# Optimization experiments

Measured on AMD Instinct MI355X. Metric: run time of the kernel, lower is better.

Reference implementation:

```python
import jax, jax.numpy as jnp
import numpy as np
from jax import lax

B, CIN, COUT, H, W = 8, 256, 128, 64, 64
KK = 9  # 3x3 kernel positions
EPS = 1e-5


def setup_inputs() -> dict:
    key = jax.random.key(0)
    ks = jax.random.split(key, 6)
    x = jax.random.normal(ks[0], (B, CIN, H, W), jnp.float32)
    # DCNv2 offset/mask conv: 3*kk channels (9 dy, 9 dx, 9 mask logits); init near zero as in DCN
    w_off = jax.random.normal(ks[1], (3 * KK, CIN, 3, 3), jnp.float32) * 0.01
    b_off = jnp.zeros((3 * KK,), jnp.float32)
    w_dcn = jax.random.normal(ks[2], (COUT, CIN, 3, 3), jnp.float32) * (1.0 / np.sqrt(CIN * 9))
    b_dcn = jnp.zeros((COUT,), jnp.float32)
    gamma1 = jnp.ones((COUT,), jnp.float32)
    beta1 = jnp.zeros((COUT,), jnp.float32)
    # torch ConvTranspose2d weight layout: [in, out, kh, kw]
    w_ct = jax.random.normal(ks[3], (COUT, COUT, 4, 4), jnp.float32) * (1.0 / np.sqrt(COUT * 16))
    gamma2 = jnp.ones((COUT,), jnp.float32)
    beta2 = jnp.zeros((COUT,), jnp.float32)
    return dict(x=x, w_off=w_off, b_off=b_off, w_dcn=w_dcn, b_dcn=b_dcn,
                gamma1=gamma1, beta1=beta1, w_ct=w_ct, gamma2=gamma2, beta2=beta2)


def _bn_relu(x, g, b):
    # BatchNorm2d (training mode: batch stats, biased var) + ReLU
    mu = jnp.mean(x, axis=(0, 2, 3), keepdims=True)
    var = jnp.var(x, axis=(0, 2, 3), keepdims=True)
    y = (x - mu) * lax.rsqrt(var + EPS) * g[None, :, None, None] + b[None, :, None, None]
    return jax.nn.relu(y)


def _forward(x, w_off, b_off, w_dcn, b_dcn, gamma1, beta1, w_ct, gamma2, beta2):
    Bx, C, Hx, Wx = x.shape
    dn = ('NCHW', 'OIHW', 'NCHW')
    # --- DCNv2: offset/mask conv (3x3, stride 1, pad 1) ---
    om = lax.conv_general_dilated(x, w_off, (1, 1), ((1, 1), (1, 1)), dimension_numbers=dn)
    om = om + b_off[None, :, None, None]
    o_y, o_x, m = om[:, :KK], om[:, KK:2 * KK], om[:, 2 * KK:]
    mask = jax.nn.sigmoid(m)  # [B,9,H,W]
    # base sampling grid: p = p0 - pad + k*dilation + offset
    ky, kx = jnp.meshgrid(jnp.arange(3, dtype=x.dtype), jnp.arange(3, dtype=x.dtype), indexing='ij')
    ky, kx = ky.reshape(KK), kx.reshape(KK)
    py = o_y + (jnp.arange(Hx, dtype=x.dtype)[None, :, None] - 1.0 + ky[:, None, None])[None]  # [B,9,H,W]
    px = o_x + (jnp.arange(Wx, dtype=x.dtype)[None, None, :] - 1.0 + kx[:, None, None])[None]
    y0 = jnp.floor(py)
    x0 = jnp.floor(px)
    ly = py - y0
    lx = px - x0
    xf = x.reshape(Bx, C, Hx * Wx)

    def corner(yi, xi, wgt):
        valid = (yi >= 0) & (yi < Hx) & (xi >= 0) & (xi < Wx)  # zero padding outside
        idx = (jnp.clip(yi, 0, Hx - 1).astype(jnp.int32) * Wx
               + jnp.clip(xi, 0, Wx - 1).astype(jnp.int32))  # [B,9,H,W]
        v = jax.vmap(lambda xb, ib: xb[:, ib])(xf, idx.reshape(Bx, -1))  # [B,C,9*H*W]
        v = v.reshape(Bx, C, KK, Hx, Wx)
        return v * (wgt * valid)[:, None]

    sampled = (corner(y0, x0, (1 - ly) * (1 - lx))
               + corner(y0, x0 + 1, (1 - ly) * lx)
               + corner(y0 + 1, x0, ly * (1 - lx))
               + corner(y0 + 1, x0 + 1, ly * lx))  # [B,C,9,H,W]
    sampled = sampled * mask[:, None]  # modulated (DCNv2)
    out = jnp.einsum('bckhw,ock->bohw', sampled, w_dcn.reshape(w_dcn.shape[0], C, KK))
    out = out + b_dcn[None, :, None, None]
    out = _bn_relu(out, gamma1, beta1)
    # --- ConvTranspose2d(k=4, s=2, p=1): conv with lhs_dilation=2, pad=k-1-p=2, flipped kernel ---
    wt = jnp.flip(w_ct, (2, 3)).transpose(1, 0, 2, 3)  # [out,in,4,4]
    out2 = lax.conv_general_dilated(out, wt, (1, 1), ((2, 2), (2, 2)),
                                    lhs_dilation=(2, 2), dimension_numbers=dn)
    return _bn_relu(out2, gamma2, beta2)  # [B,COUT,2H,2W]


def reference(x, w_off, b_off, w_dcn, b_dcn, gamma1, beta1, w_ct, gamma2, beta2):
    return _forward(x, w_off, b_off, w_dcn, b_dcn, gamma1, beta1, w_ct, gamma2, beta2)
```

## Files before the change

### kernel.cpp

```cpp
#include <hip/hip_runtime.h>
#include <stdint.h>

__device__ int   g_isf32;
__device__ float g_stats[512];

typedef __attribute__((ext_vector_type(8))) short bf16x8;
typedef __attribute__((ext_vector_type(4))) float f32x4;

__device__ __forceinline__ float bf2f(unsigned short u) {
  union { unsigned int i; float f; } v; v.i = ((unsigned int)u) << 16; return v.f;
}
__device__ __forceinline__ unsigned short f2bf(float f) {
  union { float f; unsigned int i; } v; v.f = f;
  unsigned int r = v.i + 0x7FFFu + ((v.i >> 16) & 1u);
  return (unsigned short)(r >> 16);
}
__device__ __forceinline__ unsigned int pk2(float a, float b) {
  return (unsigned int)f2bf(a) | ((unsigned int)f2bf(b) << 16);
}
__device__ __forceinline__ float ldi(const void* p, size_t i, int f) {
  return f ? ((const float*)p)[i] : bf2f(((const unsigned short*)p)[i]);
}

__global__ void k_detect(const unsigned short* __restrict__ x) {
  __shared__ int cnt;
  const int t = threadIdx.x;
  if (t == 0) cnt = 0;
  g_stats[t] = 0.f; g_stats[t + 256] = 0.f;
  __syncthreads();
  int c = 0;
  for (int j = 0; j < 16; j++) {
    unsigned short u = x[t * 16 + j];
    int e = (u >> 7) & 0xFF;
    if (e == 0xFF || (e != 0 && e <= 100)) c++;
  }
  atomicAdd(&cnt, c);
  __syncthreads();
  if (t == 0) g_isf32 = (cnt > 256) ? 1 : 0;
}

__global__ void k_prep(const void* __restrict__ w_dcn, const void* __restrict__ w_ct,
                       const void* __restrict__ w_off,
                       float* __restrict__ wdcnT, float* __restrict__ wctT,
                       float* __restrict__ woffT, unsigned short* __restrict__ wdcnA,
                       unsigned short* __restrict__ woffA) {
  const int f = g_isf32;
  int idx = blockIdx.x * 256 + threadIdx.x;
  if (idx < 294912) {
    int k = idx / 32768, c = (idx >> 7) & 255, o = idx & 127;
    wdcnT[idx] = ldi(w_dcn, (size_t)(o * 256 + c) * 9 + k, f);
  }
  int i2 = idx - 294912;
  if (i2 >= 0 && i2 < 262144) {
    int kr = i2 >> 16, kc = (i2 >> 14) & 3, i = (i2 >> 7) & 127, o = i2 & 127;
    wctT[i2] = ldi(w_ct, (size_t)((i * 128 + o) * 4 + kr) * 4 + kc, f);
  }
  int i3 = idx - (294912 + 262144);
  if (i3 >= 0 && i3 < 62208) {
    int ci = i3 / 243, r = i3 - ci * 243, k = r / 27, c = r - (r / 27) * 27;
    woffT[i3] = ldi(w_off, (size_t)(c * 256 + ci) * 9 + k, f);
  }
  int i4 = idx - 619264;
  if (i4 >= 0 && i4 < 294912) {
    int o = i4 / 2304, rem = i4 - o * 2304;
    int k = rem >> 8, c = rem & 255;
    wdcnA[i4] = f2bf(ldi(w_dcn, (size_t)(o * 256 + c) * 9 + k, f));
  }
  int i5 = idx - 914176;
  if (i5 >= 0 && i5 < 73728) {
    int m = i5 / 2304, r = i5 - m * 2304;
    int tap = r >> 8, ci = r & 255;
    float v = (m < 27) ? ldi(w_off, (size_t)(m * 256 + ci) * 9 + tap, f) : 0.f;
    woffA[i5] = f2bf(v);
  }
}

__global__ void k_prep2(const float* __restrict__ wctT, unsigned short* __restrict__ Apar) {
  int idx = blockIdx.x * 256 + threadIdx.x;
  int par = idx >> 16, rem = idx & 65535;
  int o = rem >> 9, rem2 = rem & 511;
  int tap = rem2 >> 7, i = rem2 & 127;
  int py = par >> 1, px = par & 1, a = tap >> 1, bb = tap & 1;
  int kr = (py == 0) ? (a ? 3 : 1) : (a ? 2 : 0);
  int kc = (px == 0) ? (bb ? 3 : 1) : (bb ? 2 : 0);
  Apar[idx] = f2bf(wctT[((size_t)(kr * 4 + kc) * 128 + i) * 128 + o]);
}

__global__ __launch_bounds__(256) void k_xt(const void* __restrict__ x,
                                            unsigned short* __restrict__ xT) {
  const int f = g_isf32;
  const int h = blockIdx.x, cq = blockIdx.y, b = blockIdx.z;
  const int t = threadIdx.x;
  __shared__ unsigned short T[64][72];
  {
    int cl = t >> 2, q = t & 3;
    size_t base = ((size_t)((b * 256 + cq * 64 + cl) * 64 + h) << 6) + q * 16;
    unsigned short r[16];
    if (f) {
      const float4* p = (const float4*)((const float*)x + base);
      float4 v0 = p[0], v1 = p[1], v2 = p[2], v3 = p[3];
      float vv[16] = {v0.x, v0.y, v0.z, v0.w, v1.x, v1.y, v1.z, v1.w,
                      v2.x, v2.y, v2.z, v2.w, v3.x, v3.y, v3.z, v3.w};
#pragma unroll
      for (int j = 0; j < 16; j++) r[j] = f2bf(vv[j]);
    } else {
      const unsigned short* p = (const unsigned short*)x + base;
      *(uint4*)&r[0] = *(const uint4*)p;
      *(uint4*)&r[8] = *(const uint4*)(p + 8);
    }
    *(uint4*)&T[cl][q * 16]     = *(uint4*)&r[0];
    *(uint4*)&T[cl][q * 16 + 8] = *(uint4*)&r[8];
  }
  __syncthreads();
  {
    int pl = t >> 2, qc = t & 3;
    unsigned short r[16];
#pragma unroll
    for (int j = 0; j < 16; j++) r[j] = T[qc * 16 + j][pl];
    unsigned short* op = xT + ((size_t)((b * 64 + h) * 64 + pl) << 8) + cq * 64 + qc * 16;
    *(uint4*)op       = *(uint4*)&r[0];
    *(uint4*)(op + 8) = *(uint4*)&r[8];
  }
}

__global__ __launch_bounds__(256) void k_offmfma(
    const unsigned short* __restrict__ xT,
    const unsigned short* __restrict__ woffA,
    const void* __restrict__ b_off, float* __restrict__ om) {
  const int f = g_isf32;
  const int h = blockIdx.x, b = blockIdx.y;
  const int t = threadIdx.x;
  const int wv = t >> 6, L = t & 63, quad = L >> 4, l15 = L & 15;
  __shared__ unsigned short Bs[3][66][40];
  f32x4 acc[2] = {};
  const int sl = t >> 6, sw = t & 63;

  for (int cq = 0; cq < 8; cq++) {
    __syncthreads();
    if (t < 192) {
      int row = h - 1 + sl;
      uint4 q0 = make_uint4(0, 0, 0, 0), q1 = q0, q2 = q0, q3 = q0;
      if (row >= 0 && row < 64) {
        const unsigned short* src = xT + ((size_t)((b * 64 + row) * 64 + sw) << 8) + cq * 32;
        q0 = *(const uint4*)(src);
        q1 = *(const uint4*)(src + 8);
        q2 = *(const uint4*)(src + 16);
        q3 = *(const uint4*)(src + 24);
      }
      unsigned short* d = &Bs[sl][sw + 1][0];
      *(uint4*)(d)      = q0; *(uint4*)(d + 8)  = q1;
      *(uint4*)(d + 16) = q2; *(uint4*)(d + 24) = q3;
    } else if (t < 198) {
      int idx = t - 192;
      int zs = idx >> 1, zc = (idx & 1) ? 65 : 0;
      unsigned short* d = &Bs[zs][zc][0];
      uint4 z = make_uint4(0, 0, 0, 0);
      *(uint4*)(d) = z; *(uint4*)(d + 8) = z; *(uint4*)(d + 16) = z; *(uint4*)(d + 24) = z;
    }
    __syncthreads();
#pragma unroll
    for (int tap = 0; tap < 9; tap++) {
      const int dy = tap / 3, dx = tap - dy * 3;
      const int kb = tap * 256 + cq * 32 + quad * 8;
      bf16x8 a0 = *(const bf16x8*)(woffA + (size_t)l15 * 2304 + kb);
      bf16x8 a1 = *(const bf16x8*)(woffA + (size_t)(l15 + 16) * 2304 + kb);
      bf16x8 bv = *(const bf16x8*)&Bs[dy][wv * 16 + l15 + dx][quad * 8];
      acc[0] = __builtin_amdgcn_mfma_f32_16x16x32_bf16(a0, bv, acc[0], 0, 0, 0);
      acc[1] = __builtin_amdgcn_mfma_f32_16x16x32_bf16(a1, bv, acc[1], 0, 0, 0);
    }
  }
  const int w = wv * 16 + l15;
#pragma unroll
  for (int tm = 0; tm < 2; tm++) {
#pragma unroll
    for (int r = 0; r < 4; r++) {
      int m = tm * 16 + quad * 4 + r;
      if (m < 27) {
        float bo = ldi(b_off, m, f);
        om[(size_t)((b * 27 + m) * 64 + h) * 64 + w] = acc[tm][r] + bo;
      }
    }
  }
}

__global__ __launch_bounds__(256) void k_offconv(
    const void* __restrict__ x, const void* __restrict__ b_off,
    const float* __restrict__ woffT, float* __restrict__ om) {
  const int f = g_isf32;
  const int h = blockIdx.x, b = blockIdx.y;
  const int t = threadIdx.x;
  const int cg = t & 31, wg = t >> 5;
  const int w0 = wg * 8;
  __shared__ float xs[32 * 204];
  float acc[8];
#pragma unroll
  for (int i = 0; i < 8; i++) acc[i] = 0.f;

  for (int cb = 0; cb < 256; cb += 32) {
    __syncthreads();
    for (int e = t; e < 32 * 192; e += 256) {
      int ci = e / 192, r = e - ci * 192;
      int dh = r >> 6, w = r & 63;
      int row = h + dh - 1;
      float v = 0.f;
      if (row >= 0 && row < 64)
        v = ldi(x, ((size_t)((b * 256 + cb + ci) * 64 + row) << 6) + w, f);
      xs[ci * 204 + dh * 68 + w + 1] = v;
    }
    for (int e = t; e < 96; e += 256) {
      int base = (e / 3) * 204 + (e - (e / 3) * 3) * 68;
      xs[base] = 0.f; xs[base + 65] = 0.f; xs[base + 66] = 0.f; xs[base + 67] = 0.f;
    }
    __syncthreads();

    for (int ci = 0; ci < 32; ci++) {
      float xr[3][12];
#pragma unroll
      for (int dh = 0; dh < 3; dh++) {
        const float* p = &xs[ci * 204 + dh * 68 + w0];
        float4 q0 = *(const float4*)(p);
        float4 q1 = *(const float4*)(p + 4);
        float4 q2 = *(const float4*)(p + 8);
        xr[dh][0] = q0.x; xr[dh][1] = q0.y; xr[dh][2] = q0.z; xr[dh][3] = q0.w;
        xr[dh][4] = q1.x; xr[dh][5] = q1.y; xr[dh][6] = q1.z; xr[dh][7] = q1.w;
        xr[dh][8] = q2.x; xr[dh][9] = q2.y; xr[dh][10] = q2.z; xr[dh][11] = q2.w;
      }
      if (cg < 27) {
        const float* wp = &woffT[(size_t)(cb + ci) * 243 + cg];
#pragma unroll
        for (int k = 0; k < 9; k++) {
          float wk = wp[k * 27];
          const int dh = k / 3, dx = k - (k / 3) * 3;
#pragma unroll
          for (int wi = 0; wi < 8; wi++)
            acc[wi] = fmaf(wk, xr[dh][wi + dx], acc[wi]);
        }
      }
    }
  }
  if (cg < 27) {
    float bo = ldi(b_off, cg, f);
    float* op = &om[(size_t)((b * 27 + cg) * 64 + h) * 64 + w0];
#pragma unroll
    for (int wi = 0; wi < 8; wi++) op[wi] = acc[wi] + bo;
  }
}

__global__ __launch_bounds__(256) void k_dcnf(
    const unsigned short* __restrict__ xT,
    const unsigned short* __restrict__ A,
    const float* __restrict__ om,
    const void* __restrict__ b_dcn,
    unsigned short* __restrict__ h1) {
  const int f = g_isf32;
  const int b = blockIdx.x, nt = blockIdx.y;
  const int t = threadIdx.x;
  const int wv = t >> 6, L = t & 63, quad = L >> 4, l15 = L & 15;
  const int wm = wv * 32;
  __shared__ unsigned short As[128][40];
  __shared__ unsigned short Bs[32][40];
  __shared__ float          Wg[9][32][4];
  __shared__ unsigned short Wi[9][32][4];
  f32x4 acc[2][2] = {};
  const int p0 = nt * 32;

  for (int e = t; e < 9 * 32; e += 256) {
    int k = e >> 5, p = e & 31;
    int pos = p0 + p;
    int hh = pos >> 6, ww = pos & 63;
    const float* ob = om + (size_t)(b * 27) * 4096 + pos;
    float oy = ob[(size_t)k * 4096];
    float ox = ob[(size_t)(k + 9) * 4096];
    float mm = ob[(size_t)(k + 18) * 4096];
    float msk = 1.f / (1.f + expf(-mm));
    float py = oy + (float)(hh - 1 + k / 3);
    float px = ox + (float)(ww - 1 + (k - (k / 3) * 3));
    float y0f = floorf(py), x0f = floorf(px);
    float ly = py - y0f, lx = px - x0f;
    int y0 = (int)y0f, x0 = (int)x0f;
    int y1 = y0 + 1, x1 = x0 + 1;
    float fy0 = (y0 >= 0 && y0 < 64) ? 1.f : 0.f;
    float fy1 = (y1 >= 0 && y1 < 64) ? 1.f : 0.f;
    float fx0 = (x0 >= 0 && x0 < 64) ? 1.f : 0.f;
    float fx1 = (x1 >= 0 && x1 < 64) ? 1.f : 0.f;
    int y0c = min(max(y0, 0), 63), y1c = min(max(y1, 0), 63);
    int x0c = min(max(x0, 0), 63), x1c = min(max(x1, 0), 63);
    Wg[k][p][0] = (1.f - ly) * (1.f - lx) * msk * fy0 * fx0;
    Wg[k][p][1] = (1.f - ly) * lx * msk * fy0 * fx1;
    Wg[k][p][2] = ly * (1.f - lx) * msk * fy1 * fx0;
    Wg[k][p][3] = ly * lx * msk * fy1 * fx1;
    Wi[k][p][0] = (unsigned short)(y0c * 64 + x0c);
    Wi[k][p][1] = (unsigned short)(y0c * 64 + x1c);
    Wi[k][p][2] = (unsigned short)(y1c * 64 + x0c);
    Wi[k][p][3] = (unsigned short)(y1c * 64 + x1c);
  }
  __syncthreads();

  const unsigned short* xb = xT + ((size_t)b << 20);
  const int sp = t >> 3, qc8 = t & 7;
  const int am = t >> 1, aseg = t & 1;
  const unsigned short* aprow = A + (size_t)am * 2304 + aseg * 16;

  uint4 pa0, pa1;
  uint2 pu0, pu1, pu2, pu3;
  float4 pg;

#define DCNF_ISSUE(S) {                                                   \
    int tap_ = (S) >> 3, cq_ = (S) & 7;                                   \
    int kb_ = tap_ * 256 + cq_ * 32;                                      \
    pa0 = *(const uint4*)(aprow + kb_);                                   \
    pa1 = *(const uint4*)(aprow + kb_ + 8);                               \
    pg  = *(const float4*)&Wg[tap_][sp][0];                               \
    uint2 wi2_ = *(const uint2*)&Wi[tap_][sp][0];                         \
    int i0_ = wi2_.x & 0xffff, i1_ = wi2_.x >> 16;                        \
    int i2_ = wi2_.y & 0xffff, i3_ = wi2_.y >> 16;                        \
    int cb_ = cq_ * 32 + qc8 * 4;                                         \
    pu0 = *(const uint2*)(xb + ((size_t)i0_ << 8) + cb_);                 \
    pu1 = *(const uint2*)(xb + ((size_t)i1_ << 8) + cb_);                 \
    pu2 = *(const uint2*)(xb + ((size_t)i2_ << 8) + cb_);                 \
    pu3 = *(const uint2*)(xb + ((size_t)i3_ << 8) + cb_);                 \
  }

  DCNF_ISSUE(0);
  for (int s = 0; s < 72; s++) {
    __syncthreads();
    *(uint4*)&As[am][aseg * 16]     = pa0;
    *(uint4*)&As[am][aseg * 16 + 8] = pa1;
    {
      unsigned short e0[4], e1[4], e2[4], e3[4];
      *(uint2*)e0 = pu0; *(uint2*)e1 = pu1; *(uint2*)e2 = pu2; *(uint2*)e3 = pu3;
      float g0 = pg.x, g1 = pg.y, g2 = pg.z, g3 = pg.w;
      unsigned int r[2];
#pragma unroll
      for (int j = 0; j < 2; j++) {
        float va = g0 * bf2f(e0[2 * j])     + g1 * bf2f(e1[2 * j])
                 + g2 * bf2f(e2[2 * j])     + g3 * bf2f(e3[2 * j]);
        float vb = g0 * bf2f(e0[2 * j + 1]) + g1 * bf2f(e1[2 * j + 1])
                 + g2 * bf2f(e2[2 * j + 1]) + g3 * bf2f(e3[2 * j + 1]);
        r[j] = pk2(va, vb);
      }
      *(uint2*)&Bs[sp][qc8 * 4] = make_uint2(r[0], r[1]);
    }
    if (s < 71) DCNF_ISSUE(s + 1);
    __syncthreads();
    const int ar = quad * 8;
    bf16x8 af[2], bfr[2];
#pragma unroll
    for (int tm = 0; tm < 2; tm++) af[tm]  = *(const bf16x8*)&As[wm + tm * 16 + l15][ar];
#pragma unroll
    for (int tn = 0; tn < 2; tn++) bfr[tn] = *(const bf16x8*)&Bs[tn * 16 + l15][ar];
#pragma unroll
    for (int tm = 0; tm < 2; tm++)
#pragma unroll
      for (int tn = 0; tn < 2; tn++)
        acc[tm][tn] = __builtin_amdgcn_mfma_f32_16x16x32_bf16(af[tm], bfr[tn], acc[tm][tn], 0, 0, 0);
  }
#undef DCNF_ISSUE

#pragma unroll
  for (int tm = 0; tm < 2; tm++) {
#pragma unroll
    for (int r = 0; r < 4; r++) {
      int m = wm + tm * 16 + quad * 4 + r;
      float bd = ldi(b_dcn, m, f);
#pragma unroll
      for (int tn = 0; tn < 2; tn++) {
        float v = acc[tm][tn][r] + bd;
        int n = p0 + tn * 16 + l15;
        h1[(size_t)(b * 128 + m) * 4096 + n] = f2bf(v);
      }
    }
  }
}

__global__ __launch_bounds__(256) void k_stats1(const unsigned short* __restrict__ h1) {
  const int m = blockIdx.x, b = blockIdx.y;
  const int t = threadIdx.x;
  const unsigned short* p = h1 + (size_t)(b * 128 + m) * 4096 + t * 16;
  uint4 q0 = *(const uint4*)p;
  uint4 q1 = *(const uint4*)(p + 8);
  unsigned short e[16];
  *(uint4*)&e[0] = q0; *(uint4*)&e[8] = q1;
  float s = 0.f, q = 0.f;
#pragma unroll
  for (int j = 0; j < 16; j++) { float v = bf2f(e[j]); s += v; q += v * v; }
#pragma unroll
  for (int msk = 1; msk < 64; msk <<= 1) {
    s += __shfl_xor(s, msk, 64);
    q += __shfl_xor(q, msk, 64);
  }
  if ((t & 63) == 0) { atomicAdd(&g_stats[m], s); atomicAdd(&g_stats[128 + m], q); }
}

__global__ __launch_bounds__(256) void k_dcn(
    const void* __restrict__ x, const float* __restrict__ om,
    const float* __restrict__ wdcnT, const void* __restrict__ b_dcn,
    unsigned short* __restrict__ h1) {
  const int f = g_isf32;
  const int h = blockIdx.x, b = blockIdx.y;
  const int t = threadIdx.x;
  __shared__ float S[64 * 64];
  __shared__ int   midx[64][4];
  __shared__ float mwgt[64][4];
  const int og = t >> 4, pg = t & 15;
  const int pA = t & 63, cgA = t >> 6;
  float acc[8][4];
#pragma unroll
  for (int j = 0; j < 8; j++)
#pragma unroll
    for (int i = 0; i < 4; i++) acc[j][i] = 0.f;

  for (int k = 0; k < 9; k++) {
    if (t < 64) {
      const int w = t;
      const float* ob = &om[(size_t)(b * 27) * 4096 + h * 64 + w];
      float oy = ob[(size_t)k * 4096];
      float ox = ob[(size_t)(k + 9) * 4096];
      float mm = ob[(size_t)(k + 18) * 4096];
      float msk = 1.f / (1.f + expf(-mm));
      float py = oy + (float)(h - 1 + k / 3);
      float px = ox + (float)(w - 1 + (k - (k / 3) * 3));
      float y0f = floorf(py), x0f = floorf(px);
      float ly = py - y0f, lx = px - x0f;
      int y0 = (int)y0f, x0 = (int)x0f;
      int y1 = y0 + 1, x1 = x0 + 1;
      float fy0 = (y0 >= 0 && y0 < 64) ? 1.f : 0.f;
      float fy1 = (y1 >= 0 && y1 < 64) ? 1.f : 0.f;
      float fx0 = (x0 >= 0 && x0 < 64) ? 1.f : 0.f;
      float fx1 = (x1 >= 0 && x1 < 64) ? 1.f : 0.f;
      int y0c = min(max(y0, 0), 63), y1c = min(max(y1, 0), 63);
      int x0c = min(max(x0, 0), 63), x1c = min(max(x1, 0), 63);
      midx[w][0] = y0c * 64 + x0c;
      midx[w][1] = y0c * 64 + x1c;
      midx[w][2] = y1c * 64 + x0c;
      midx[w][3] = y1c * 64 + x1c;
      mwgt[w][0] = (1.f - ly) * (1.f - lx) * msk * fy0 * fx0;
      mwgt[w][1] = (1.f - ly) * lx * msk * fy0 * fx1;
      mwgt[w][2] = ly * (1.f - lx) * msk * fy1 * fx0;
      mwgt[w][3] = ly * lx * msk * fy1 * fx1;
    }
    for (int ch = 0; ch < 4; ch++) {
      __syncthreads();
      {
        const int i0 = midx[pA][0], i1 = midx[pA][1], i2 = midx[pA][2], i3 = midx[pA][3];
        const float g0 = mwgt[pA][0], g1 = mwgt[pA][1], g2 = mwgt[pA][2], g3 = mwgt[pA][3];
        const size_t cbase = (size_t)(b * 256 + ch * 64 + cgA * 16) * 4096;
        float* Sp = &S[(cgA * 16) * 64 + pA];
#pragma unroll 4
        for (int j = 0; j < 16; j++) {
          const size_t xo = cbase + (size_t)j * 4096;
          float v = g0 * ldi(x, xo + i0, f) + g1 * ldi(x, xo + i1, f)
                  + g2 * ldi(x, xo + i2, f) + g3 * ldi(x, xo + i3, f);
          Sp[j * 64] = v;
        }
      }
      __syncthreads();
      const float* wk = wdcnT + (size_t)k * 32768 + (size_t)(ch * 64) * 128;
#pragma unroll 2
      for (int c2 = 0; c2 < 64; c2++) {
        float4 a0 = *(const float4*)&wk[c2 * 128 + og * 8];
        float4 a1 = *(const float4*)&wk[c2 * 128 + og * 8 + 4];
        float4 s4 = *(const float4*)&S[c2 * 64 + pg * 4];
        float aa[8] = {a0.x, a0.y, a0.z, a0.w, a1.x, a1.y, a1.z, a1.w};
        float ss[4] = {s4.x, s4.y, s4.z, s4.w};
#pragma unroll
        for (int j = 0; j < 8; j++)
#pragma unroll
          for (int i = 0; i < 4; i++)
            acc[j][i] = fmaf(aa[j], ss[i], acc[j][i]);
      }
    }
  }
#pragma unroll
  for (int j = 0; j < 8; j++) {
    const int o = og * 8 + j;
    float bd = ldi(b_dcn, o, f);
    float v0 = acc[j][0] + bd, v1 = acc[j][1] + bd, v2 = acc[j][2] + bd, v3 = acc[j][3] + bd;
    float s = v0 + v1 + v2 + v3;
    float q = v0 * v0 + v1 * v1 + v2 * v2 + v3 * v3;
    uint2 pkv = make_uint2(pk2(v0, v1), pk2(v2, v3));
    *(uint2*)(h1 + (size_t)((b * 128 + o) * 64 + h) * 64 + pg * 4) = pkv;
#pragma unroll
    for (int m = 1; m < 16; m <<= 1) {
      s += __shfl_xor(s, m, 64);
      q += __shfl_xor(q, m, 64);
    }
    if (pg == 0) { atomicAdd(&g_stats[o], s); atomicAdd(&g_stats[128 + o], q); }
  }
}

__global__ __launch_bounds__(256) void k_bn1t(
    const unsigned short* __restrict__ h1, const void* __restrict__ g1,
    const void* __restrict__ be1, unsigned short* __restrict__ h1T) {
  const int f = g_isf32;
  const int pt = blockIdx.x, chh = blockIdx.y, b = blockIdx.z;
  const int t = threadIdx.x;
  __shared__ unsigned short T[64][72];
  const int c0 = chh * 64, p0 = pt * 64;
  {
    int cl = t >> 2, q = t & 3;
    int o = c0 + cl;
    float mu = g_stats[o] * (1.f / 32768.f);
    float var = g_stats[128 + o] * (1.f / 32768.f) - mu * mu;
    float sc = rsqrtf(var + 1e-5f) * ldi(g1, o, f);
    float sh = ldi(be1, o, f) - mu * sc;
    const unsigned short* hp = h1 + (size_t)(b * 128 + o) * 4096 + p0 + q * 16;
    uint4 q0 = *(const uint4*)hp, q1 = *(const uint4*)(hp + 8);
    unsigned short e[16], r[16];
    *(uint4*)&e[0] = q0; *(uint4*)&e[8] = q1;
#pragma unroll
    for (int j = 0; j < 16; j++)
      r[j] = f2bf(fmaxf(fmaf(bf2f(e[j]), sc, sh), 0.f));
    *(uint4*)&T[cl][q * 16]     = *(uint4*)&r[0];
    *(uint4*)&T[cl][q * 16 + 8] = *(uint4*)&r[8];
  }
  __syncthreads();
  {
    int pl = t >> 2, qc = t & 3;
    unsigned short r[16];
#pragma unroll
    for (int j = 0; j < 16; j++) r[j] = T[qc * 16 + j][pl];
    unsigned short* op = h1T + (size_t)(b * 4096 + p0 + pl) * 128 + c0 + qc * 16;
    *(uint4*)op       = *(uint4*)&r[0];
    *(uint4*)(op + 8) = *(uint4*)&r[8];
  }
}

__global__ void k_bn1(unsigned short* __restrict__ h1, const void* __restrict__ g1,
                      const void* __restrict__ be1) {
  const int f = g_isf32;
  int gid = blockIdx.x * 256 + threadIdx.x;
  size_t base = (size_t)gid * 8;
  int o = (int)((base >> 12) & 127);
  float mu = g_stats[o] * (1.f / 32768.f);
  float var = g_stats[128 + o] * (1.f / 32768.f) - mu * mu;
  float sc = rsqrtf(var + 1e-5f) * ldi(g1, o, f);
  float sh = ldi(be1, o, f) - mu * sc;
  uint4 p = *(const uint4*)(h1 + base);
  unsigned int pp[4] = {p.x, p.y, p.z, p.w};
  unsigned int r[4];
#pragma unroll
  for (int i = 0; i < 4; i++) {
    float f0 = fmaxf(fmaf(bf2f((unsigned short)(pp[i] & 0xffff)), sc, sh), 0.f);
    float f1 = fmaxf(fmaf(bf2f((unsigned short)(pp[i] >> 16)), sc, sh), 0.f);
    r[i] = pk2(f0, f1);
  }
  *(uint4*)(h1 + base) = make_uint4(r[0], r[1], r[2], r[3]);
}

__global__ __launch_bounds__(256) void k_ctgemm(
    const unsigned short* __restrict__ h1T,
    const unsigned short* __restrict__ Apar,
    void* __restrict__ out2p) {
  const int f = g_isf32;
  const int nt = blockIdx.x, par = blockIdx.y, b = blockIdx.z;
  const int py = par >> 1, px = par & 1;
  const int t = threadIdx.x;
  const int wv = t >> 6, L = t & 63;
  const int quad = L >> 4, l15 = L & 15;
  const int wm = (wv >> 1) * 64, wn = (wv & 1) * 64;
  __shared__ unsigned short As[128][40];
  __shared__ unsigned short Bs[128][40];
  f32x4 acc[4][4] = {};
  const int y0 = nt * 2;
  const unsigned short* Ap = Apar + (size_t)par * 128 * 512;
  const unsigned short* hb = h1T + (size_t)b * 4096 * 128;
  const int sp = t >> 1, shalf = t & 1;
  const int srr = sp >> 6, sx = sp & 63;

  for (int kk = 0; kk < 512; kk += 32) {
    const int tap = kk >> 7, ic = kk & 127;
    const int a = tap >> 1, bb = tap & 1;
    const int ya = (py == 0) ? (a ? -1 : 0) : (a ? 0 : 1);
    const int xb = (px == 0) ? (bb ? -1 : 0) : (bb ? 0 : 1);
    __syncthreads();
    {
      int m = t >> 1, seg = t & 1;
      const unsigned short* ap = Ap + (size_t)m * 512 + kk + seg * 16;
      uint4 q0 = *(const uint4*)(ap);
      uint4 q1 = *(const uint4*)(ap + 8);
      *(uint4*)&As[m][seg * 16]     = q0;
      *(uint4*)&As[m][seg * 16 + 8] = q1;
    }
    {
      int srcy = y0 + srr + ya;
      int srcx = sx + xb;
      uint4 q0 = make_uint4(0, 0, 0, 0), q1 = q0;
      if (srcy >= 0 && srcy < 64 && srcx >= 0 && srcx < 64) {
        const unsigned short* hp = hb + ((size_t)(srcy * 64 + srcx)) * 128 + ic + shalf * 16;
        q0 = *(const uint4*)(hp);
        q1 = *(const uint4*)(hp + 8);
      }
      *(uint4*)&Bs[sp][shalf * 16]     = q0;
      *(uint4*)&Bs[sp][shalf * 16 + 8] = q1;
    }
    __syncthreads();
    const int ar = quad * 8;
    bf16x8 af[4], bfr[4];
#pragma unroll
    for (int tm = 0; tm < 4; tm++) af[tm]  = *(const bf16x8*)&As[wm + tm * 16 + l15][ar];
#pragma unroll
    for (int tn = 0; tn < 4; tn++) bfr[tn] = *(const bf16x8*)&Bs[wn + tn * 16 + l15][ar];
#pragma unroll
    for (int tm = 0; tm < 4; tm++)
#pragma unroll
      for (int tn = 0; tn < 4; tn++)
        acc[tm][tn] = __builtin_amdgcn_mfma_f32_16x16x32_bf16(af[tm], bfr[tn], acc[tm][tn], 0, 0, 0);
  }

  const size_t obase = (size_t)((par * 8 + b) * 128) * 4096;
#pragma unroll
  for (int tm = 0; tm < 4; tm++) {
#pragma unroll
    for (int r = 0; r < 4; r++) {
      int m = wm + tm * 16 + quad * 4 + r;
#pragma unroll
      for (int tn = 0; tn < 4; tn++) {
        float v = acc[tm][tn][r];
        int n = wn + tn * 16 + l15;
        size_t ofs = obase + (size_t)m * 4096 + (size_t)((y0 + (n >> 6)) * 64 + (n & 63));
        if (f) ((float*)out2p)[ofs] = v;
        else   ((unsigned short*)out2p)[ofs] = f2bf(v);
      }
    }
  }
}

__global__ __launch_bounds__(256) void k_stats2(const void* __restrict__ out2p) {
  const int f = g_isf32;
  const int m = blockIdx.x, pb = blockIdx.y;
  const int t = threadIdx.x;
  size_t base = ((size_t)pb * 128 + m) * 4096 + (size_t)t * 16;
  float s = 0.f, q = 0.f;
  if (f) {
    const float* p = (const float*)out2p + base;
#pragma unroll
    for (int j = 0; j < 4; j++) {
      float4 v = *(const float4*)(p + j * 4);
      s += v.x + v.y + v.z + v.w;
      q += v.x * v.x + v.y * v.y + v.z * v.z + v.w * v.w;
    }
  } else {
    const unsigned short* p = (const unsigned short*)out2p + base;
    uint4 q0 = *(const uint4*)p, q1 = *(const uint4*)(p + 8);
    unsigned short e[16];
    *(uint4*)&e[0] = q0; *(uint4*)&e[8] = q1;
#pragma unroll
    for (int j = 0; j < 16; j++) { float v = bf2f(e[j]); s += v; q += v * v; }
  }
#pragma unroll
  for (int msk = 1; msk < 64; msk <<= 1) {
    s += __shfl_xor(s, msk, 64);
    q += __shfl_xor(q, msk, 64);
  }
  if ((t & 63) == 0) { atomicAdd(&g_stats[256 + m], s); atomicAdd(&g_stats[384 + m], q); }
}

__global__ __launch_bounds__(256) void k_bn2f(
    const void* __restrict__ out2p, const void* __restrict__ g2,
    const void* __restrict__ be2, void* __restrict__ out) {
  const int f = g_isf32;
  const int m = blockIdx.x, b = blockIdx.y;
  const int t = threadIdx.x;
  float mu = g_stats[256 + m] * (1.f / 131072.f);
  float var = g_stats[384 + m] * (1.f / 131072.f) - mu * mu;
  float sc = rsqrtf(var + 1e-5f) * ldi(g2, m, f);
  float sh = ldi(be2, m, f) - mu * sc;
  const int row8 = t >> 3, xseg = t & 7;
  const int xh0 = xseg * 8;
#pragma unroll
  for (int pss = 0; pss < 4; pss++) {
    int yy = pss * 32 + row8;
    int y = yy >> 1, py = yy & 1;
    size_t s0 = ((size_t)((py * 2 + 0) * 8 + b) * 128 + m) * 4096 + (size_t)(y * 64 + xh0);
    size_t s1 = ((size_t)((py * 2 + 1) * 8 + b) * 128 + m) * 4096 + (size_t)(y * 64 + xh0);
    float v0[8], v1[8];
    if (f) {
      const float* p0 = (const float*)out2p + s0;
      const float* p1 = (const float*)out2p + s1;
      float4 a0 = *(const float4*)p0, a1 = *(const float4*)(p0 + 4);
      float4 c0 = *(const float4*)p1, c1 = *(const float4*)(p1 + 4);
      v0[0] = a0.x; v0[1] = a0.y; v0[2] = a0.z; v0[3] = a0.w;
      v0[4] = a1.x; v0[5] = a1.y; v0[6] = a1.z; v0[7] = a1.w;
      v1[0] = c0.x; v1[1] = c0.y; v1[2] = c0.z; v1[3] = c0.w;
      v1[4] = c1.x; v1[5] = c1.y; v1[6] = c1.z; v1[7] = c1.w;
    } else {
      const unsigned short* p0 = (const unsigned short*)out2p + s0;
      const unsigned short* p1 = (const unsigned short*)out2p + s1;
      uint4 u0 = *(const uint4*)p0, u1 = *(const uint4*)p1;
      unsigned short e0[8], e1[8];
      *(uint4*)&e0[0] = u0; *(uint4*)&e1[0] = u1;
#pragma unroll
      for (int j = 0; j < 8; j++) { v0[j] = bf2f(e0[j]); v1[j] = bf2f(e1[j]); }
    }
    float r[16];
#pragma unroll
    for (int i = 0; i < 8; i++) {
      r[2 * i]     = fmaxf(fmaf(v0[i], sc, sh), 0.f);
      r[2 * i + 1] = fmaxf(fmaf(v1[i], sc, sh), 0.f);
    }
    size_t ob = (size_t)(b * 128 + m) * 16384 + (size_t)yy * 128 + (size_t)(xh0 * 2);
    if (f) {
      float* op = (float*)out + ob;
#pragma unroll
      for (int v4 = 0; v4 < 4; v4++)
        ((float4*)op)[v4] = make_float4(r[4 * v4], r[4 * v4 + 1], r[4 * v4 + 2], r[4 * v4 + 3]);
    } else {
      unsigned short* op = (unsigned short*)out + ob;
      unsigned int w_[8];
#pragma unroll
      for (int i = 0; i < 8; i++) w_[i] = pk2(r[2 * i], r[2 * i + 1]);
      *(uint4*)(op)     = make_uint4(w_[0], w_[1], w_[2], w_[3]);
      *(uint4*)(op + 8) = make_uint4(w_[4], w_[5], w_[6], w_[7]);
    }
  }
}

__global__ __launch_bounds__(256) void k_ctconv(
    const unsigned short* __restrict__ h1n, const float* __restrict__ wctT,
    void* __restrict__ out2) {
  const int f = g_isf32;
  const int y = blockIdx.x, b = blockIdx.y;
  const int t = threadIdx.x;
  const int og = t >> 3, xg = t & 7;
  __shared__ float hs[2 * 32 * 68];
  int kr0, kr1, r0, r1;
  if ((y & 1) == 0) { kr0 = 1; r0 = y >> 1; kr1 = 3; r1 = (y >> 1) - 1; }
  else              { kr0 = 0; r0 = (y + 1) >> 1; kr1 = 2; r1 = (y - 1) >> 1; }
  float acc[4][16];
#pragma unroll
  for (int j = 0; j < 4; j++)
#pragma unroll
    for (int i = 0; i < 16; i++) acc[j][i] = 0.f;

  for (int ihc = 0; ihc < 4; ihc++) {
    __syncthreads();
    for (int e = t; e < 2 * 32 * 64; e += 256) {
      int rr = e >> 11, rem = e & 2047, il = rem >> 6, w = rem & 63;
      int i = ihc * 32 + il;
      int row = rr ? r1 : r0;
      float v = 0.f;
      if (row >= 0 && row < 64)
        v = bf2f(h1n[(size_t)((b * 128 + i) * 64 + row) * 64 + w]);
      hs[(rr * 32 + il) * 68 + w + 1] = v;
    }
    for (int e = t; e < 64; e += 256) {
      int base = e * 68;
      hs[base] = 0.f; hs[base + 65] = 0.f; hs[base + 66] = 0.f; hs[base + 67] = 0.f;
    }
    __syncthreads();
    for (int il = 0; il < 32; il++) {
      const int i = ihc * 32 + il;
      float br[2][12];
#pragma unroll
      for (int rr = 0; rr < 2; rr++) {
        const float* p = &hs[(rr * 32 + il) * 68 + xg * 8];
        float4 q0 = *(const float4*)(p);
        float4 q1 = *(const float4*)(p + 4);
        float4 q2 = *(const float4*)(p + 8);
        br[rr][0] = q0.x; br[rr][1] = q0.y; br[rr][2] = q0.z; br[rr][3] = q0.w;
        br[rr][4] = q1.x; br[rr][5] = q1.y; br[rr][6] = q1.z; br[rr][7] = q1.w;
        br[rr][8] = q2.x; br[rr][9] = q2.y; br[rr][10] = q2.z; br[rr][11] = q2.w;
      }
      float a[2][4][4];
#pragma unroll
      for (int rr = 0; rr < 2; rr++) {
        const int krr = rr ? kr1 : kr0;
#pragma unroll
        for (int kc = 0; kc < 4; kc++) {
          float4 av = *(const float4*)&wctT[((size_t)(krr * 4 + kc) * 128 + i) * 128 + og * 4];
          a[rr][kc][0] = av.x; a[rr][kc][1] = av.y; a[rr][kc][2] = av.z; a[rr][kc][3] = av.w;
        }
      }
#pragma unroll
      for (int xi = 0; xi < 16; xi++) {
        const int u = xi >> 1;
        const int kcA = (xi & 1) ? 0 : 1;
        const int lwA = (xi & 1) ? u + 2 : u + 1;
        const int kcB = (xi & 1) ? 2 : 3;
        const int lwB = (xi & 1) ? u + 1 : u;
#pragma unroll
        for (int rr = 0; rr < 2; rr++) {
#pragma unroll
          for (int j = 0; j < 4; j++) {
            acc[j][xi] = fmaf(a[rr][kcA][j], br[rr][lwA], acc[j][xi]);
            acc[j][xi] = fmaf(a[rr][kcB][j], br[rr][lwB], acc[j][xi]);
          }
        }
      }
    }
  }
#pragma unroll
  for (int j = 0; j < 4; j++) {
    const int o = og * 4 + j;
    float s = 0.f, q = 0.f;
#pragma unroll
    for (int xi = 0; xi < 16; xi++) { s += acc[j][xi]; q += acc[j][xi] * acc[j][xi]; }
    size_t ofs = (size_t)((b * 128 + o) * 128 + y) * 128 + xg * 16;
    if (f) {
      float* op = (float*)out2 + ofs;
#pragma unroll
      for (int v4 = 0; v4 < 4; v4++)
        ((float4*)op)[v4] = make_float4(acc[j][4 * v4], acc[j][4 * v4 + 1],
                                        acc[j][4 * v4 + 2], acc[j][4 * v4 + 3]);
    } else {
      unsigned int w_[8];
#pragma unroll
      for (int xi = 0; xi < 8; xi++) w_[xi] = pk2(acc[j][2 * xi], acc[j][2 * xi + 1]);
      unsigned short* op = (unsigned short*)out2 + ofs;
      *(uint4*)(op)     = make_uint4(w_[0], w_[1], w_[2], w_[3]);
      *(uint4*)(op + 8) = make_uint4(w_[4], w_[5], w_[6], w_[7]);
    }
#pragma unroll
    for (int m = 1; m < 8; m <<= 1) {
      s += __shfl_xor(s, m, 64);
      q += __shfl_xor(q, m, 64);
    }
    if (xg == 0) { atomicAdd(&g_stats[256 + o], s); atomicAdd(&g_stats[384 + o], q); }
  }
}

__global__ void k_bn2(void* __restrict__ out2, const void* __restrict__ g2,
                      const void* __restrict__ be2) {
  const int f = g_isf32;
  int gid = blockIdx.x * 256 + threadIdx.x;
  size_t base = (size_t)gid * 8;
  int o = (int)((base >> 14) & 127);
  float mu = g_stats[256 + o] * (1.f / 131072.f);
  float var = g_stats[384 + o] * (1.f / 131072.f) - mu * mu;
  float sc = rsqrtf(var + 1e-5f) * ldi(g2, o, f);
  float sh = ldi(be2, o, f) - mu * sc;
  if (f) {
    float4* op = (float4*)out2 + gid * 2;
    float4 p0 = op[0], p1 = op[1];
    p0.x = fmaxf(fmaf(p0.x, sc, sh), 0.f); p0.y = fmaxf(fmaf(p0.y, sc, sh), 0.f);
    p0.z = fmaxf(fmaf(p0.z, sc, sh), 0.f); p0.w = fmaxf(fmaf(p0.w, sc, sh), 0.f);
    p1.x = fmaxf(fmaf(p1.x, sc, sh), 0.f); p1.y = fmaxf(fmaf(p1.y, sc, sh), 0.f);
    p1.z = fmaxf(fmaf(p1.z, sc, sh), 0.f); p1.w = fmaxf(fmaf(p1.w, sc, sh), 0.f);
    op[0] = p0; op[1] = p1;
  } else {
    unsigned short* ob = (unsigned short*)out2 + base;
    uint4 p = *(const uint4*)ob;
    unsigned int pp[4] = {p.x, p.y, p.z, p.w};
    unsigned int r[4];
#pragma unroll
    for (int i = 0; i < 4; i++) {
      float f0 = fmaxf(fmaf(bf2f((unsigned short)(pp[i] & 0xffff)), sc, sh), 0.f);
      float f1 = fmaxf(fmaf(bf2f((unsigned short)(pp[i] >> 16)), sc, sh), 0.f);
      r[i] = pk2(f0, f1);
    }
    *(uint4*)ob = make_uint4(r[0], r[1], r[2], r[3]);
  }
}

extern "C" void kernel_launch(void* const* d_in, const int* in_sizes, int n_in,
                              void* d_out, int out_size, void* d_ws, size_t ws_size,
                              hipStream_t stream) {
  const void* x     = d_in[0];
  const void* w_off = d_in[1];
  const void* b_off = d_in[2];
  const void* w_dcn = d_in[3];
  const void* b_dcn = d_in[4];
  const void* g1    = d_in[5];
  const void* be1   = d_in[6];
  const void* w_ct  = d_in[7];
  const void* g2    = d_in[8];
  const void* be2   = d_in[9];

  char* ws = (char*)d_ws;
  const bool fast = ws_size >= (size_t)166000000;

  unsigned short* h1; float* om; float* wdcnT; float* wctT;
  float* woffT; unsigned short* wdcnA; unsigned short* AparB; unsigned short* h1T;
  void* out2p; unsigned short* xT; unsigned short* woffA;
  if (fast) {
    xT    = (unsigned short*)(ws + 0);
    h1    = (unsigned short*)(ws + 16777216);
    h1T   = (unsigned short*)(ws + 25165824);
    out2p = (void*)(ws + 33554432);
    om    = (float*)(ws + 100663296);
    wctT  = (float*)(ws + 104202240);
    AparB = (unsigned short*)(ws + 105250816);
    wdcnA = (unsigned short*)(ws + 105775104);
    woffA = (unsigned short*)(ws + 106364928);
    woffT = (float*)(ws + 106512384);
    wdcnT = (float*)(ws + 106761216);
  } else {
    h1    = (unsigned short*)(ws + 0);
    om    = (float*)(ws + 8388608);
    wdcnT = (float*)(ws + 11927552);
    wctT  = (float*)(ws + 13107200);
    woffT = (float*)(ws + 14155776);
    wdcnA = (unsigned short*)(ws + 14404608);
    woffA = (unsigned short*)(ws + 14994432);
    AparB = nullptr;
    h1T   = nullptr;
    out2p = nullptr;
    xT    = nullptr;
  }

  k_detect<<<dim3(1), 256, 0, stream>>>((const unsigned short*)x);
  k_prep<<<dim3(3859), 256, 0, stream>>>(w_dcn, w_ct, w_off, wdcnT, wctT, woffT, wdcnA, woffA);
  if (fast) {
    k_xt<<<dim3(64, 4, 8), 256, 0, stream>>>(x, xT);
    k_offmfma<<<dim3(64, 8), 256, 0, stream>>>(xT, woffA, b_off, om);
    k_prep2<<<dim3(1024), 256, 0, stream>>>(wctT, AparB);
    k_dcnf<<<dim3(8, 128), 256, 0, stream>>>(xT, wdcnA, om, b_dcn, h1);
    k_stats1<<<dim3(128, 8), 256, 0, stream>>>(h1);
    k_bn1t<<<dim3(64, 2, 8), 256, 0, stream>>>(h1, g1, be1, h1T);
    k_ctgemm<<<dim3(32, 4, 8), 256, 0, stream>>>(h1T, AparB, out2p);
    k_stats2<<<dim3(128, 32), 256, 0, stream>>>(out2p);
    k_bn2f<<<dim3(128, 8), 256, 0, stream>>>(out2p, g2, be2, d_out);
  } else {
    k_offconv<<<dim3(64, 8), 256, 0, stream>>>(x, b_off, woffT, om);
    k_dcn<<<dim3(64, 8), 256, 0, stream>>>(x, om, wdcnT, b_dcn, h1);
    k_bn1<<<dim3(2048), 256, 0, stream>>>(h1, g1, be1);
    k_ctconv<<<dim3(128, 8), 256, 0, stream>>>(h1, wctT, d_out);
    k_bn2<<<dim3(8192), 256, 0, stream>>>(d_out, g2, be2);
  }
}
```

Baseline: 372.7 us.

## Double-buffer DCN sampled tile and load weight fragments directly to registers

Replaces the single-buffered LDS staging of the A (weight) tile with direct global-to-register loads in MFMA fragment layout, and double-buffers the bilinear-sampled B tile in LDS. The main loop drops from two barriers per K-step to one, and the gather/combine for the next step now overlaps the current MFMAs. The cost is more registers for the prefetched fragments and uncoalesced per-lane global loads of A, which each wave now fetches separately instead of sharing through LDS.

```diff
diff --git a/kernel.cpp b/kernel.cpp
--- a/kernel.cpp
+++ b/kernel.cpp
@@ -257,8 +257,7 @@
   const int t = threadIdx.x;
   const int wv = t >> 6, L = t & 63, quad = L >> 4, l15 = L & 15;
   const int wm = wv * 32;
-  __shared__ unsigned short As[128][40];
-  __shared__ unsigned short Bs[32][40];
+  __shared__ unsigned short Bs[2][32][40];
   __shared__ float          Wg[9][32][4];
   __shared__ unsigned short Wi[9][32][4];
   f32x4 acc[2][2] = {};
@@ -298,18 +297,18 @@
 
   const unsigned short* xb = xT + ((size_t)b << 20);
   const int sp = t >> 3, qc8 = t & 7;
-  const int am = t >> 1, aseg = t & 1;
-  const unsigned short* aprow = A + (size_t)am * 2304 + aseg * 16;
-
-  uint4 pa0, pa1;
+  const unsigned short* arow0 = A + (size_t)(wm + l15) * 2304 + quad * 8;
+  const unsigned short* arow1 = A + (size_t)(wm + 16 + l15) * 2304 + quad * 8;
+
+  bf16x8 pa0, pa1, a0c, a1c;
   uint2 pu0, pu1, pu2, pu3;
   float4 pg;
 
 #define DCNF_ISSUE(S) {                                                   \
     int tap_ = (S) >> 3, cq_ = (S) & 7;                                   \
     int kb_ = tap_ * 256 + cq_ * 32;                                      \
-    pa0 = *(const uint4*)(aprow + kb_);                                   \
-    pa1 = *(const uint4*)(aprow + kb_ + 8);                               \
+    pa0 = *(const bf16x8*)(arow0 + kb_);                                  \
+    pa1 = *(const bf16x8*)(arow1 + kb_);                                  \
     pg  = *(const float4*)&Wg[tap_][sp][0];                               \
     uint2 wi2_ = *(const uint2*)&Wi[tap_][sp][0];                         \
     int i0_ = wi2_.x & 0xffff, i1_ = wi2_.x >> 16;                        \
@@ -321,41 +320,52 @@
     pu3 = *(const uint2*)(xb + ((size_t)i3_ << 8) + cb_);                 \
   }
 
+#define DCNF_COMBINE(BUF) {                                               \
+    unsigned short e0[4], e1[4], e2[4], e3[4];                            \
+    *(uint2*)e0 = pu0; *(uint2*)e1 = pu1;                                 \
+    *(uint2*)e2 = pu2; *(uint2*)e3 = pu3;                                 \
+    float g0 = pg.x, g1 = pg.y, g2 = pg.z, g3 = pg.w;                     \
+    unsigned int r0_, r1_;                                                \
+    {                                                                     \
+      float va = g0 * bf2f(e0[0]) + g1 * bf2f(e1[0])                      \
+               + g2 * bf2f(e2[0]) + g3 * bf2f(e3[0]);                     \
+      float vb = g0 * bf2f(e0[1]) + g1 * bf2f(e1[1])                      \
+               + g2 * bf2f(e2[1]) + g3 * bf2f(e3[1]);                     \
+      r0_ = pk2(va, vb);                                                  \
+    }                                                                     \
+    {                                                                     \
+      float va = g0 * bf2f(e0[2]) + g1 * bf2f(e1[2])                      \
+               + g2 * bf2f(e2[2]) + g3 * bf2f(e3[2]);                     \
+      float vb = g0 * bf2f(e0[3]) + g1 * bf2f(e1[3])                      \
+               + g2 * bf2f(e2[3]) + g3 * bf2f(e3[3]);                     \
+      r1_ = pk2(va, vb);                                                  \
+    }                                                                     \
+    *(uint2*)&Bs[BUF][sp][qc8 * 4] = make_uint2(r0_, r1_);                \
+  }
+
   DCNF_ISSUE(0);
+  a0c = pa0; a1c = pa1;
+  DCNF_COMBINE(0);
+  DCNF_ISSUE(1);
+  __syncthreads();
+
   for (int s = 0; s < 72; s++) {
+    const int cur = s & 1;
+    bf16x8 b0 = *(const bf16x8*)&Bs[cur][l15][quad * 8];
+    bf16x8 b1 = *(const bf16x8*)&Bs[cur][16 + l15][quad * 8];
+    acc[0][0] = __builtin_amdgcn_mfma_f32_16x16x32_bf16(a0c, b0, acc[0][0], 0, 0, 0);
+    acc[0][1] = __builtin_amdgcn_mfma_f32_16x16x32_bf16(a0c, b1, acc[0][1], 0, 0, 0);
+    acc[1][0] = __builtin_amdgcn_mfma_f32_16x16x32_bf16(a1c, b0, acc[1][0], 0, 0, 0);
+    acc[1][1] = __builtin_amdgcn_mfma_f32_16x16x32_bf16(a1c, b1, acc[1][1], 0, 0, 0);
+    if (s < 71) {
+      a0c = pa0; a1c = pa1;
+      DCNF_COMBINE(cur ^ 1);
+      if (s < 70) DCNF_ISSUE(s + 2);
+    }
     __syncthreads();
-    *(uint4*)&As[am][aseg * 16]     = pa0;
-    *(uint4*)&As[am][aseg * 16 + 8] = pa1;
-    {
-      unsigned short e0[4], e1[4], e2[4], e3[4];
-      *(uint2*)e0 = pu0; *(uint2*)e1 = pu1; *(uint2*)e2 = pu2; *(uint2*)e3 = pu3;
-      float g0 = pg.x, g1 = pg.y, g2 = pg.z, g3 = pg.w;
-      unsigned int r[2];
-#pragma unroll
-      for (int j = 0; j < 2; j++) {
-        float va = g0 * bf2f(e0[2 * j])     + g1 * bf2f(e1[2 * j])
-                 + g2 * bf2f(e2[2 * j])     + g3 * bf2f(e3[2 * j]);
-        float vb = g0 * bf2f(e0[2 * j + 1]) + g1 * bf2f(e1[2 * j + 1])
-                 + g2 * bf2f(e2[2 * j + 1]) + g3 * bf2f(e3[2 * j + 1]);
-        r[j] = pk2(va, vb);
-      }
-      *(uint2*)&Bs[sp][qc8 * 4] = make_uint2(r[0], r[1]);
-    }
-    if (s < 71) DCNF_ISSUE(s + 1);
-    __syncthreads();
-    const int ar = quad * 8;
-    bf16x8 af[2], bfr[2];
-#pragma unroll
-    for (int tm = 0; tm < 2; tm++) af[tm]  = *(const bf16x8*)&As[wm + tm * 16 + l15][ar];
-#pragma unroll
-    for (int tn = 0; tn < 2; tn++) bfr[tn] = *(const bf16x8*)&Bs[tn * 16 + l15][ar];
-#pragma unroll
-    for (int tm = 0; tm < 2; tm++)
-#pragma unroll
-      for (int tn = 0; tn < 2; tn++)
-        acc[tm][tn] = __builtin_amdgcn_mfma_f32_16x16x32_bf16(af[tm], bfr[tn], acc[tm][tn], 0, 0, 0);
   }
 #undef DCNF_ISSUE
+#undef DCNF_COMBINE
 
 #pragma unroll
   for (int tm = 0; tm < 2; tm++) {
```

Measured after the change: 397.4 us. 1.07x slower.
